# Performance work log

Measured on AMD Instinct MI355X. Metric: run time of the kernel, lower is better.

Reference implementation:

```python
import jax, jax.numpy as jnp
import numpy as np

DIM = 768
NUM_HEADS = 12
N_TOKENS = 4096


def setup_inputs() -> dict:
    key = jax.random.key(0)
    k_x, k_qkv, k_proj, k_pb = jax.random.split(key, 4)
    x = jax.random.normal(k_x, (N_TOKENS, DIM), dtype=jnp.float32)
    # nn.Linear(dim, dim*3, bias=False): weight shape (3*dim, dim)
    w_qkv = jax.random.normal(k_qkv, (3 * DIM, DIM), dtype=jnp.float32) * (DIM ** -0.5)
    # nn.Linear(dim, dim): weight (dim, dim), bias (dim,)
    w_proj = jax.random.normal(k_proj, (DIM, DIM), dtype=jnp.float32) * (DIM ** -0.5)
    b_proj = jax.random.normal(k_pb, (DIM,), dtype=jnp.float32) * 0.01
    return {"x": x, "w_qkv": w_qkv, "w_proj": w_proj, "b_proj": b_proj}


def reference(x, w_qkv, w_proj, b_proj):
    N, C = x.shape
    H = NUM_HEADS
    hd = C // H
    scale = hd ** -0.5
    qkv = (x @ w_qkv.T).reshape(N, 3, H, hd)  # (N, 3, H, hd)
    q = qkv[:, 0]  # (N, H, hd)
    k = qkv[:, 1]
    v = qkv[:, 2]
    # full NxN score matrix per head, as in the original (non-flash) code
    attn = jnp.einsum("nhd,mhd->hnm", q, k) * scale  # (H, N, N)
    attn = jax.nn.softmax(attn, axis=-1)
    out = jnp.einsum("hnm,mhd->nhd", attn, v).reshape(N, C)  # (N, C)
    return out @ w_proj.T + b_proj
```

## Files before the change

kernel.cpp:

```cpp
#include <hip/hip_runtime.h>
#include <hip/hip_bf16.h>

typedef __bf16 bf16_t;
typedef __attribute__((ext_vector_type(8))) __bf16 bf16x8;
typedef __attribute__((ext_vector_type(4))) __bf16 bf16x4;
typedef __attribute__((ext_vector_type(4))) short s16x4;
typedef __attribute__((ext_vector_type(4))) float f32x4;
typedef __attribute__((ext_vector_type(4))) _Float16 f16x4;

#define NTOK 4096
#define DIM  768
#define NH   12
#define HD   64
#define NSPLIT 4
#define KHALF (NTOK / NSPLIT)
#define XSZ  (NTOK * DIM)
#define WQSZ (3 * DIM * DIM)
#define WPSZ (DIM * DIM)
#define SCALE_L2E 0.18033688011112042f
#define SOFTMAX_C 12.0f

__device__ __forceinline__ bf16x8 load8(const bf16_t* p) {
    return *reinterpret_cast<const bf16x8*>(p);
}
__device__ __forceinline__ void store8(bf16_t* p, bf16x8 v) {
    *reinterpret_cast<bf16x8*>(p) = v;
}
__device__ __forceinline__ void gl2lds16(const bf16_t* g, bf16_t* l) {
    __builtin_amdgcn_global_load_lds(
        (const __attribute__((address_space(1))) void*)g,
        (__attribute__((address_space(3))) void*)l, 16, 0, 0);
}

__global__ __launch_bounds__(256) void cvt_kernel(
    const float* __restrict__ x, const float* __restrict__ wq,
    const float* __restrict__ wp,
    bf16_t* __restrict__ xb, bf16_t* __restrict__ wqb, bf16_t* __restrict__ wpb)
{
    size_t i = ((size_t)blockIdx.x * 256 + threadIdx.x) * 4;
    const float* src; bf16_t* dst; size_t off;
    if (i < XSZ)             { src = x;  dst = xb;  off = i; }
    else if (i < XSZ + WQSZ) { src = wq; dst = wqb; off = i - XSZ; }
    else                     { src = wp; dst = wpb; off = i - XSZ - WQSZ; }
    float4 v = *reinterpret_cast<const float4*>(src + off);
    bf16x4 o = { (bf16_t)v.x, (bf16_t)v.y, (bf16_t)v.z, (bf16_t)v.w };
    *reinterpret_cast<bf16x4*>(dst + off) = o;
}

__global__ __launch_bounds__(256) void qkv_gemm_kernel(
    const bf16_t* __restrict__ X, const bf16_t* __restrict__ W,
    bf16_t* __restrict__ Qo, bf16_t* __restrict__ Ko, bf16_t* __restrict__ Vt)
{
    __shared__ __align__(16) bf16_t As[128 * 32];
    __shared__ __align__(16) bf16_t Bs[128 * 32];
    const int tid  = threadIdx.x;
    const int wave = tid >> 6, lane = tid & 63;
    const int lr = lane & 15, lq = lane >> 4;
    const int M0 = blockIdx.x * 128;
    const int N0 = blockIdx.y * 128;
    const int wm = (wave >> 1) * 64, wn = (wave & 1) * 64;

    const int g_row = wave * 32 + (lane >> 2);
    const int g_col = (lane & 3) * 8;

    f32x4 acc[4][4] = {};

    for (int k0 = 0; k0 < DIM; k0 += 32) {
        #pragma unroll
        for (int c = 0; c < 2; ++c) {
            gl2lds16(&X[(size_t)(M0 + g_row + c * 16) * DIM + k0 + g_col],
                     &As[(wave * 32 + c * 16) * 32]);
            gl2lds16(&W[(size_t)(N0 + g_row + c * 16) * DIM + k0 + g_col],
                     &Bs[(wave * 32 + c * 16) * 32]);
        }
        __syncthreads();
        bf16x8 af[4], bfr[4];
        #pragma unroll
        for (int i = 0; i < 4; ++i) af[i]  = load8(&As[(wm + i * 16 + lr) * 32 + lq * 8]);
        #pragma unroll
        for (int i = 0; i < 4; ++i) bfr[i] = load8(&Bs[(wn + i * 16 + lr) * 32 + lq * 8]);
        #pragma unroll
        for (int r = 0; r < 4; ++r)
            #pragma unroll
            for (int c = 0; c < 4; ++c)
                acc[r][c] = __builtin_amdgcn_mfma_f32_16x16x32_bf16(af[r], bfr[c], acc[r][c], 0, 0, 0);
        __syncthreads();
    }

    const int t = N0 / DIM;
    if (t == 2) {
        #pragma unroll
        for (int r = 0; r < 4; ++r)
            #pragma unroll
            for (int c = 0; c < 4; ++c) {
                int m0 = M0 + wm + r * 16 + lq * 4;
                int rem = N0 + wn + c * 16 + lr - 2 * DIM;
                int hh = rem >> 6, d = rem & 63;
                bf16x4 v = { (bf16_t)acc[r][c][0], (bf16_t)acc[r][c][1],
                             (bf16_t)acc[r][c][2], (bf16_t)acc[r][c][3] };
                *reinterpret_cast<bf16x4*>(&Vt[((size_t)hh * HD + d) * NTOK + m0]) = v;
            }
    } else {
        #pragma unroll
        for (int r = 0; r < 4; ++r)
            #pragma unroll
            for (int c = 0; c < 4; ++c)
                #pragma unroll
                for (int reg = 0; reg < 4; ++reg) {
                    int m = M0 + wm + r * 16 + lq * 4 + reg;
                    int rem = N0 + wn + c * 16 + lr - t * DIM;
                    int hh = rem >> 6, d = rem & 63;
                    float v = acc[r][c][reg];
                    if (t == 0) Qo[(hh * NTOK + m) * HD + d] = (bf16_t)(v * SCALE_L2E);
                    else        Ko[(hh * NTOK + m) * HD + d] = (bf16_t)v;
                }
    }
}

__global__ __launch_bounds__(256) void flash_attn_kernel(
    const bf16_t* __restrict__ Qb, const bf16_t* __restrict__ Kb,
    const bf16_t* __restrict__ Vtb, _Float16* __restrict__ Opart,
    float* __restrict__ Lpart)
{
    __shared__ __align__(16) bf16_t Ks[2][64 * 64];
    __shared__ __align__(16) bf16_t Vs[2][64 * 64];
    const int tid  = threadIdx.x;
    const int wave = tid >> 6, lane = tid & 63;
    const int lr = lane & 15, lq = lane >> 4;
    const int h  = blockIdx.y;
    const int q0 = blockIdx.x * 128;
    const int sp = blockIdx.z;
    const int kt0 = sp * KHALF;
    const int NIT = KHALF / 64;

    const int kc0 = (lq ^ (lr & 7)) * 8;
    const int kc1 = ((4 + lq) ^ (lr & 7)) * 8;
    int vc[4];
    #pragma unroll
    for (int g = 0; g < 4; ++g)
        vc[g] = ((2 * g + (lq >> 1)) ^ (lr & 7)) * 8 + (lq & 1) * 4;

    const int srow = lane >> 3;
    const int scol = ((lane & 7) ^ srow) * 8;
    const bf16_t* kbase = &Kb[(size_t)h * NTOK * HD];
    const bf16_t* vbase = &Vtb[(size_t)h * HD * NTOK];
    const size_t kofA = (size_t)(wave * 16 + srow) * HD + scol;
    const size_t kofB = kofA + (size_t)8 * HD;
    const size_t vofA = (size_t)(wave * 16 + srow) * NTOK + scol;
    const size_t vofB = vofA + (size_t)8 * NTOK;
    const int ldA = (wave * 16) * 64;
    const int ldB = (wave * 16 + 8) * 64;

    const bf16_t* qrowA = &Qb[((size_t)h * NTOK + q0 + wave * 32 + lr) * HD];
    const bf16_t* qrowB = qrowA + 16 * HD;
    bf16x8 qa0 = load8(&qrowA[lq * 8]);
    bf16x8 qa1 = load8(&qrowA[32 + lq * 8]);
    bf16x8 qb0 = load8(&qrowB[lq * 8]);
    bf16x8 qb1 = load8(&qrowB[32 + lq * 8]);

    float la = 0.f, lb = 0.f;
    f32x4 oA[4] = {}, oB[4] = {};
    const f32x4 mc = { -SOFTMAX_C, -SOFTMAX_C, -SOFTMAX_C, -SOFTMAX_C };

    {
        const bf16_t* kp = kbase + (size_t)kt0 * HD;
        const bf16_t* vp = vbase + kt0;
        gl2lds16(kp + kofA, &Ks[0][ldA]);
        gl2lds16(kp + kofB, &Ks[0][ldB]);
        gl2lds16(vp + vofA, &Vs[0][ldA]);
        gl2lds16(vp + vofB, &Vs[0][ldB]);
    }
    __syncthreads();

    for (int it = 0; it < NIT; ++it) {
        const int buf = it & 1;

        if (it + 1 < NIT) {
            const int kn = kt0 + (it + 1) * 64;
            const bf16_t* kp = kbase + (size_t)kn * HD;
            const bf16_t* vp = vbase + kn;
            gl2lds16(kp + kofA, &Ks[buf ^ 1][ldA]);
            gl2lds16(kp + kofB, &Ks[buf ^ 1][ldB]);
            gl2lds16(vp + vofA, &Vs[buf ^ 1][ldA]);
            gl2lds16(vp + vofB, &Vs[buf ^ 1][ldB]);
        }

        #pragma unroll
        for (int g = 0; g < 4; ++g) {
            bf16x8 k0 = load8(&Ks[buf][(g * 16 + lr) * 64 + kc0]);
            bf16x8 k1 = load8(&Ks[buf][(g * 16 + lr) * 64 + kc1]);
            f32x4 za = mc, zb = mc;
            __builtin_amdgcn_s_setprio(1);
            za = __builtin_amdgcn_mfma_f32_16x16x32_bf16(k0, qa0, za, 0, 0, 0);
            za = __builtin_amdgcn_mfma_f32_16x16x32_bf16(k1, qa1, za, 0, 0, 0);
            zb = __builtin_amdgcn_mfma_f32_16x16x32_bf16(k0, qb0, zb, 0, 0, 0);
            zb = __builtin_amdgcn_mfma_f32_16x16x32_bf16(k1, qb1, zb, 0, 0, 0);
            __builtin_amdgcn_s_setprio(0);
            #pragma unroll
            for (int r = 0; r < 4; ++r) {
                za[r] = __builtin_amdgcn_exp2f(za[r]);
                la += za[r];
                zb[r] = __builtin_amdgcn_exp2f(zb[r]);
                lb += zb[r];
            }
            bf16x4 pa = { (bf16_t)za[0], (bf16_t)za[1],
                          (bf16_t)za[2], (bf16_t)za[3] };
            bf16x4 pb = { (bf16_t)zb[0], (bf16_t)zb[1],
                          (bf16_t)zb[2], (bf16_t)zb[3] };
            s16x4 psa = __builtin_bit_cast(s16x4, pa);
            s16x4 psb = __builtin_bit_cast(s16x4, pb);
            __builtin_amdgcn_s_setprio(1);
            #pragma unroll
            for (int dt = 0; dt < 4; ++dt) {
                s16x4 va = *reinterpret_cast<const s16x4*>(
                    &Vs[buf][(dt * 16 + lr) * 64 + vc[g]]);
                oA[dt] = __builtin_amdgcn_mfma_f32_16x16x16bf16_1k(va, psa, oA[dt], 0, 0, 0);
                oB[dt] = __builtin_amdgcn_mfma_f32_16x16x16bf16_1k(va, psb, oB[dt], 0, 0, 0);
            }
            __builtin_amdgcn_s_setprio(0);
        }

        __syncthreads();
    }

    la += __shfl_xor(la, 16); la += __shfl_xor(la, 32);
    lb += __shfl_xor(lb, 16); lb += __shfl_xor(lb, 32);
    const int ma = q0 + wave * 32 + lr;
    const int mb = ma + 16;
    if (lq == 0) {
        Lpart[((size_t)sp * NH + h) * NTOK + ma] = la;
        Lpart[((size_t)sp * NH + h) * NTOK + mb] = lb;
    }
    _Float16* oa = &Opart[((size_t)sp * NTOK + ma) * DIM + h * HD];
    _Float16* ob = &Opart[((size_t)sp * NTOK + mb) * DIM + h * HD];
    #pragma unroll
    for (int dt = 0; dt < 4; ++dt) {
        f16x4 va = { (_Float16)oA[dt][0], (_Float16)oA[dt][1],
                     (_Float16)oA[dt][2], (_Float16)oA[dt][3] };
        f16x4 vb = { (_Float16)oB[dt][0], (_Float16)oB[dt][1],
                     (_Float16)oB[dt][2], (_Float16)oB[dt][3] };
        *reinterpret_cast<f16x4*>(&oa[dt * 16 + lq * 4]) = va;
        *reinterpret_cast<f16x4*>(&ob[dt * 16 + lq * 4]) = vb;
    }
}

__global__ __launch_bounds__(256) void combine_kernel(
    const _Float16* __restrict__ Opart, const float* __restrict__ Lpart,
    bf16_t* __restrict__ Ab)
{
    int idx = blockIdx.x * 256 + threadIdx.x;
    int m = idx / (DIM / 4);
    int c = (idx - m * (DIM / 4)) * 4;
    int hh = c >> 6;
    float l = 0.f;
    #pragma unroll
    for (int s = 0; s < NSPLIT; ++s)
        l += Lpart[((size_t)s * NH + hh) * NTOK + m];
    float rv = 1.f / l;
    float a0 = 0.f, a1 = 0.f, a2 = 0.f, a3 = 0.f;
    #pragma unroll
    for (int s = 0; s < NSPLIT; ++s) {
        f16x4 v = *reinterpret_cast<const f16x4*>(
            &Opart[((size_t)s * NTOK + m) * DIM + c]);
        a0 += (float)v[0]; a1 += (float)v[1];
        a2 += (float)v[2]; a3 += (float)v[3];
    }
    bf16x4 o = { (bf16_t)(a0 * rv), (bf16_t)(a1 * rv),
                 (bf16_t)(a2 * rv), (bf16_t)(a3 * rv) };
    *reinterpret_cast<bf16x4*>(&Ab[(size_t)m * DIM + c]) = o;
}

__global__ __launch_bounds__(256) void proj_gemm_kernel(
    const bf16_t* __restrict__ A, const bf16_t* __restrict__ W,
    const float* __restrict__ bias, float* __restrict__ out)
{
    __shared__ __align__(16) bf16_t As[64 * 32];
    __shared__ __align__(16) bf16_t Bs[64 * 32];
    const int tid  = threadIdx.x;
    const int wave = tid >> 6, lane = tid & 63;
    const int lr = lane & 15, lq = lane >> 4;
    const int M0 = blockIdx.x * 64;
    const int N0 = blockIdx.y * 64;
    const int wr = (wave >> 1) * 32, wc = (wave & 1) * 32;
    const int g_row = tid >> 2;
    const int g_col = (tid & 3) * 8;

    f32x4 acc[2][2] = {};

    for (int k0 = 0; k0 < DIM; k0 += 32) {
        gl2lds16(&A[(size_t)(M0 + g_row) * DIM + k0 + g_col], &As[wave * 512]);
        gl2lds16(&W[(size_t)(N0 + g_row) * DIM + k0 + g_col], &Bs[wave * 512]);
        __syncthreads();
        bf16x8 a0 = load8(&As[(wr + lr) * 32 + lq * 8]);
        bf16x8 a1 = load8(&As[(wr + 16 + lr) * 32 + lq * 8]);
        bf16x8 b0 = load8(&Bs[(wc + lr) * 32 + lq * 8]);
        bf16x8 b1 = load8(&Bs[(wc + 16 + lr) * 32 + lq * 8]);
        acc[0][0] = __builtin_amdgcn_mfma_f32_16x16x32_bf16(a0, b0, acc[0][0], 0, 0, 0);
        acc[0][1] = __builtin_amdgcn_mfma_f32_16x16x32_bf16(a0, b1, acc[0][1], 0, 0, 0);
        acc[1][0] = __builtin_amdgcn_mfma_f32_16x16x32_bf16(a1, b0, acc[1][0], 0, 0, 0);
        acc[1][1] = __builtin_amdgcn_mfma_f32_16x16x32_bf16(a1, b1, acc[1][1], 0, 0, 0);
        __syncthreads();
    }

    #pragma unroll
    for (int r = 0; r < 2; ++r)
        #pragma unroll
        for (int c = 0; c < 2; ++c)
            #pragma unroll
            for (int reg = 0; reg < 4; ++reg) {
                int m = M0 + wr + r * 16 + lq * 4 + reg;
                int n = N0 + wc + c * 16 + lr;
                out[(size_t)m * DIM + n] = acc[r][c][reg] + bias[n];
            }
}

extern "C" void kernel_launch(void* const* d_in, const int* in_sizes, int n_in,
                              void* d_out, int out_size, void* d_ws, size_t ws_size,
                              hipStream_t stream)
{
    const float* x      = (const float*)d_in[0];
    const float* w_qkv  = (const float*)d_in[1];
    const float* w_proj = (const float*)d_in[2];
    const float* b_proj = (const float*)d_in[3];
    float* out = (float*)d_out;

    char* ws = (char*)d_ws;
    const size_t sz = (size_t)NH * NTOK * HD * sizeof(bf16_t);
    bf16_t*   Q     = (bf16_t*)(ws);
    bf16_t*   K     = (bf16_t*)(ws + sz);
    bf16_t*   Vt    = (bf16_t*)(ws + 2 * sz);
    bf16_t*   xb    = (bf16_t*)(ws + 3 * sz);
    bf16_t*   wqb   = (bf16_t*)(ws + 3 * sz + (size_t)XSZ * 2);
    bf16_t*   wpb   = (bf16_t*)(ws + 3 * sz + (size_t)(XSZ + WQSZ) * 2);
    _Float16* Opart = (_Float16*)(ws + 3 * sz + (size_t)(XSZ + WQSZ + WPSZ) * 2);
    float*    Lpart = (float*)xb;
    bf16_t*   Ab    = Q;

    cvt_kernel<<<dim3((XSZ + WQSZ + WPSZ) / 1024), 256, 0, stream>>>(
        x, w_qkv, w_proj, xb, wqb, wpb);
    qkv_gemm_kernel<<<dim3(NTOK / 128, (3 * DIM) / 128), 256, 0, stream>>>(
        xb, wqb, Q, K, Vt);
    flash_attn_kernel<<<dim3(NTOK / 128, NH, NSPLIT), 256, 0, stream>>>(
        Q, K, Vt, Opart, Lpart);
    combine_kernel<<<dim3((NTOK * DIM / 4) / 256), 256, 0, stream>>>(
        Opart, Lpart, Ab);
    proj_gemm_kernel<<<dim3(NTOK / 64, DIM / 64), 256, 0, stream>>>(
        Ab, wpb, b_proj, out);
}
```

Baseline: 187.7 us.

## Double attention block to 8 waves and compute softmax row sums via MFMA

The flash attention block grows from 4 to 8 waves covering 256 query rows, so each K/V tile staged in LDS is shared by twice as many queries and each thread issues half as many global-to-LDS loads. The row-sum of exponentials is now accumulated with an extra MFMA against a ones vector instead of scalar adds plus cross-lane shuffles. This moves VALU work onto the matrix unit and cuts K/V traffic, but the grid has half as many blocks, which may hurt occupancy and load balance. The row sums are also now taken from bf16-rounded probabilities rather than fp32 values.

```diff
diff --git a/kernel.cpp b/kernel.cpp
--- a/kernel.cpp
+++ b/kernel.cpp
@@ -117,7 +117,7 @@
     }
 }
 
-__global__ __launch_bounds__(256) void flash_attn_kernel(
+__global__ __launch_bounds__(512) void flash_attn_kernel(
     const bf16_t* __restrict__ Qb, const bf16_t* __restrict__ Kb,
     const bf16_t* __restrict__ Vtb, _Float16* __restrict__ Opart,
     float* __restrict__ Lpart)
@@ -128,7 +128,7 @@
     const int wave = tid >> 6, lane = tid & 63;
     const int lr = lane & 15, lq = lane >> 4;
     const int h  = blockIdx.y;
-    const int q0 = blockIdx.x * 128;
+    const int q0 = blockIdx.x * 256;
     const int sp = blockIdx.z;
     const int kt0 = sp * KHALF;
     const int NIT = KHALF / 64;
@@ -144,12 +144,9 @@
     const int scol = ((lane & 7) ^ srow) * 8;
     const bf16_t* kbase = &Kb[(size_t)h * NTOK * HD];
     const bf16_t* vbase = &Vtb[(size_t)h * HD * NTOK];
-    const size_t kofA = (size_t)(wave * 16 + srow) * HD + scol;
-    const size_t kofB = kofA + (size_t)8 * HD;
-    const size_t vofA = (size_t)(wave * 16 + srow) * NTOK + scol;
-    const size_t vofB = vofA + (size_t)8 * NTOK;
-    const int ldA = (wave * 16) * 64;
-    const int ldB = (wave * 16 + 8) * 64;
+    const size_t kof = (size_t)(wave * 8 + srow) * HD + scol;
+    const size_t vof = (size_t)(wave * 8 + srow) * NTOK + scol;
+    const int ldw = (wave * 8) * 64;
 
     const bf16_t* qrowA = &Qb[((size_t)h * NTOK + q0 + wave * 32 + lr) * HD];
     const bf16_t* qrowB = qrowA + 16 * HD;
@@ -158,18 +155,14 @@
     bf16x8 qb0 = load8(&qrowB[lq * 8]);
     bf16x8 qb1 = load8(&qrowB[32 + lq * 8]);
 
-    float la = 0.f, lb = 0.f;
     f32x4 oA[4] = {}, oB[4] = {};
+    f32x4 lsA = {}, lsB = {};
     const f32x4 mc = { -SOFTMAX_C, -SOFTMAX_C, -SOFTMAX_C, -SOFTMAX_C };
-
-    {
-        const bf16_t* kp = kbase + (size_t)kt0 * HD;
-        const bf16_t* vp = vbase + kt0;
-        gl2lds16(kp + kofA, &Ks[0][ldA]);
-        gl2lds16(kp + kofB, &Ks[0][ldB]);
-        gl2lds16(vp + vofA, &Vs[0][ldA]);
-        gl2lds16(vp + vofB, &Vs[0][ldB]);
-    }
+    const short ONE = (short)0x3F80;
+    const s16x4 ones = { ONE, ONE, ONE, ONE };
+
+    gl2lds16(kbase + (size_t)kt0 * HD + kof, &Ks[0][ldw]);
+    gl2lds16(vbase + kt0 + vof,              &Vs[0][ldw]);
     __syncthreads();
 
     for (int it = 0; it < NIT; ++it) {
@@ -177,12 +170,8 @@
 
         if (it + 1 < NIT) {
             const int kn = kt0 + (it + 1) * 64;
-            const bf16_t* kp = kbase + (size_t)kn * HD;
-            const bf16_t* vp = vbase + kn;
-            gl2lds16(kp + kofA, &Ks[buf ^ 1][ldA]);
-            gl2lds16(kp + kofB, &Ks[buf ^ 1][ldB]);
-            gl2lds16(vp + vofA, &Vs[buf ^ 1][ldA]);
-            gl2lds16(vp + vofB, &Vs[buf ^ 1][ldB]);
+            gl2lds16(kbase + (size_t)kn * HD + kof, &Ks[buf ^ 1][ldw]);
+            gl2lds16(vbase + kn + vof,              &Vs[buf ^ 1][ldw]);
         }
 
         #pragma unroll
@@ -199,9 +188,7 @@
             #pragma unroll
             for (int r = 0; r < 4; ++r) {
                 za[r] = __builtin_amdgcn_exp2f(za[r]);
-                la += za[r];
                 zb[r] = __builtin_amdgcn_exp2f(zb[r]);
-                lb += zb[r];
             }
             bf16x4 pa = { (bf16_t)za[0], (bf16_t)za[1],
                           (bf16_t)za[2], (bf16_t)za[3] };
@@ -210,6 +197,8 @@
             s16x4 psa = __builtin_bit_cast(s16x4, pa);
             s16x4 psb = __builtin_bit_cast(s16x4, pb);
             __builtin_amdgcn_s_setprio(1);
+            lsA = __builtin_amdgcn_mfma_f32_16x16x16bf16_1k(ones, psa, lsA, 0, 0, 0);
+            lsB = __builtin_amdgcn_mfma_f32_16x16x16bf16_1k(ones, psb, lsB, 0, 0, 0);
             #pragma unroll
             for (int dt = 0; dt < 4; ++dt) {
                 s16x4 va = *reinterpret_cast<const s16x4*>(
@@ -223,8 +212,7 @@
         __syncthreads();
     }
 
-    la += __shfl_xor(la, 16); la += __shfl_xor(la, 32);
-    lb += __shfl_xor(lb, 16); lb += __shfl_xor(lb, 32);
+    const float la = lsA[0], lb = lsB[0];
     const int ma = q0 + wave * 32 + lr;
     const int mb = ma + 16;
     if (lq == 0) {
@@ -340,7 +328,7 @@
         x, w_qkv, w_proj, xb, wqb, wpb);
     qkv_gemm_kernel<<<dim3(NTOK / 128, (3 * DIM) / 128), 256, 0, stream>>>(
         xb, wqb, Q, K, Vt);
-    flash_attn_kernel<<<dim3(NTOK / 128, NH, NSPLIT), 256, 0, stream>>>(
+    flash_attn_kernel<<<dim3(NTOK / 256, NH, NSPLIT), 512, 0, stream>>>(
         Q, K, Vt, Opart, Lpart);
     combine_kernel<<<dim3((NTOK * DIM / 4) / 256), 256, 0, stream>>>(
         Opart, Lpart, Ab);
```

Measured after the change: 187.5 us. Within noise of the previous version (-0.1%).
